# Kernel optimization log

Hardware: AMD Instinct MI355X
Metric: run time of the kernel (lower is better)

Reference implementation:

```python
import jax, jax.numpy as jnp
import numpy as np

B, L, E, H = 4, 2048, 1024, 16
HD = E // H  # 64
ROPE_BASE = 10000.0


def setup_inputs() -> dict:
    key = jax.random.key(0)
    ks = jax.random.split(key, 4)
    x = jax.random.normal(ks[0], (B, L, E), dtype=jnp.float32)
    Wqkv = jax.random.normal(ks[1], (3 * E, E), dtype=jnp.float32) * (E ** -0.5)
    bqkv = jnp.zeros((3 * E,), dtype=jnp.float32)
    Wout = jax.random.normal(ks[2], (E, E), dtype=jnp.float32) * (E ** -0.5)
    bout = jnp.zeros((E,), dtype=jnp.float32)
    # RoPE tables: (1, 1, L, HD/2)
    half = HD // 2
    inv_freq = 1.0 / (ROPE_BASE ** (jnp.arange(half, dtype=jnp.float32) / half))
    t = jnp.arange(L, dtype=jnp.float32)
    freqs = t[:, None] * inv_freq[None, :]  # (L, half)
    cos = jnp.cos(freqs)[None, None]
    sin = jnp.sin(freqs)[None, None]
    return {"x": x, "cos": cos, "sin": sin, "Wqkv": Wqkv, "bqkv": bqkv,
            "Wout": Wout, "bout": bout}


def _apply_rope(q, k, cos, sin):
    half = q.shape[-1] // 2
    q1, q2 = q[..., :half], q[..., half:]
    k1, k2 = k[..., :half], k[..., half:]
    q_rot = jnp.concatenate([q1 * cos - q2 * sin, q1 * sin + q2 * cos], axis=-1)
    k_rot = jnp.concatenate([k1 * cos - k2 * sin, k1 * sin + k2 * cos], axis=-1)
    return q_rot, k_rot


def reference(x, cos, sin, Wqkv, bqkv, Wout, bout):
    b, l, e = x.shape
    qkv = x @ Wqkv.T + bqkv  # (B, L, 3E)
    q, k, v = jnp.split(qkv, 3, axis=-1)
    # (B, H, L, HD)
    q = q.reshape(b, l, H, HD).transpose(0, 2, 1, 3)
    k = k.reshape(b, l, H, HD).transpose(0, 2, 1, 3)
    v = v.reshape(b, l, H, HD).transpose(0, 2, 1, 3)
    q, k = _apply_rope(q, k, cos, sin)
    scale = 1.0 / jnp.sqrt(jnp.asarray(HD, dtype=x.dtype))
    scores = jnp.einsum('bhqd,bhkd->bhqk', q, k) * scale
    attn = jax.nn.softmax(scores, axis=-1)
    out = jnp.einsum('bhqk,bhkd->bhqd', attn, v)  # (B, H, L, HD)
    out = out.transpose(0, 2, 1, 3).reshape(b, l, e)
    out = out @ Wout.T + bout
    return out
```

## Files before the change

### kernel.cpp

```cpp
#include <hip/hip_runtime.h>
#include <math.h>

#define B 4
#define L 2048
#define E 1024
#define H 16
#define HD 64
#define MROWS (B*L)
#define E3 (3*E)

using bf16x8   = __attribute__((ext_vector_type(8))) short;
using f16x8    = __attribute__((ext_vector_type(8))) _Float16;
using floatx4  = __attribute__((ext_vector_type(4))) float;
using floatx16 = __attribute__((ext_vector_type(16))) float;

__device__ inline ushort f2bf(float x) {
    uint u = __float_as_uint(x);
    u += 0x7FFF + ((u >> 16) & 1);
    return (ushort)(u >> 16);
}
__device__ inline float bf2f(ushort h) { return __uint_as_float(((uint)h) << 16); }
__device__ inline ushort f2h(float x) { _Float16 h = (_Float16)x; return *(ushort*)&h; }

#if __has_builtin(__builtin_amdgcn_exp2f)
#define EXP2F(x) __builtin_amdgcn_exp2f(x)
#else
#define EXP2F(x) exp2f(x)
#endif

__device__ inline void async16(const void* g, void* l) {
    __builtin_amdgcn_global_load_lds(
        (const __attribute__((address_space(1))) uint*)g,
        (__attribute__((address_space(3))) uint*)l, 16, 0, 0);
}

__device__ inline uint pack_rtz(float odd, float even) {
    return __builtin_amdgcn_perm(__float_as_uint(odd), __float_as_uint(even), 0x07060302u);
}

#define VMW(n)  asm volatile("s_waitcnt vmcnt(" #n ")" ::: "memory")
#define LGKM0() asm volatile("s_waitcnt lgkmcnt(0)" ::: "memory")
#define SBAR()  __builtin_amdgcn_s_barrier()
#define SCHED0() __builtin_amdgcn_sched_barrier(0)

#define N1Q ((size_t)MROWS * E / 4)
#define N2Q ((size_t)E3 * E / 4)
#define N3Q ((size_t)E * E / 4)
__global__ __launch_bounds__(256) void cvt_all(
        const float* __restrict__ x, const float* __restrict__ wq,
        const float* __restrict__ wo, ushort* __restrict__ x16,
        ushort* __restrict__ wq16, ushort* __restrict__ wo16)
{
    size_t i = (size_t)blockIdx.x * 256 + threadIdx.x;
    const float* src; ushort* dst; size_t j;
    if (i < N1Q)                  { src = x;  dst = x16;  j = i; }
    else if (i < N1Q + N2Q)       { src = wq; dst = wq16; j = i - N1Q; }
    else                          { src = wo; dst = wo16; j = i - N1Q - N2Q; }
    float4 v = ((const float4*)src)[j];
    ushort4 o;
    o.x = f2h(v.x); o.y = f2h(v.y); o.z = f2h(v.z); o.w = f2h(v.w);
    ((ushort4*)dst)[j] = o;
}

template<int MODE>
__global__ __launch_bounds__(256, 2) void gemm4w(
        const ushort* __restrict__ A16, const ushort* __restrict__ B16,
        const float* __restrict__ bias, float* __restrict__ Cf,
        ushort* __restrict__ qh, ushort* __restrict__ kh, ushort* __restrict__ vT,
        const float* __restrict__ cosT, const float* __restrict__ sinT,
        int Ndim, int Kdim)
{
    constexpr int BM    = 256;
    constexpr int ACOLS = BM * 32;
    constexpr int SLOT  = ACOLS + 4096;
    __shared__ ushort lds[3][SLOT];

    const int tid  = threadIdx.x;
    const int w    = tid >> 6, lane = tid & 63;
    const int g    = lane >> 4, c = lane & 15;
    const int wm   = w >> 1,  wn = w & 1;

    const int gx  = gridDim.x;
    const int nwg = gx * gridDim.y;
    int bid = blockIdx.y * gx + blockIdx.x;
    bid = (bid & 7) * (nwg >> 3) + (bid >> 3);
    const int m0 = (bid / gx) * BM;
    const int n0 = (bid % gx) * 128;

    const int rl = lane >> 2, q = lane & 3;
    const ushort* srcA[4]; int dstA[4];
#pragma unroll
    for (int p = 0; p < 4; ++p) {
        const int row = (w * 4 + p) * 16 + rl;
        const int kg  = q ^ ((row >> 1) & 3);
        srcA[p] = A16 + (size_t)(m0 + row) * Kdim + kg * 8;
        dstA[p] = (w * 4 + p) * 512;
    }
    const ushort* srcB[2]; int dstB[2];
#pragma unroll
    for (int p = 0; p < 2; ++p) {
        const int n  = (w * 2 + p) * 16 + rl;
        const int kg = q ^ ((n >> 1) & 3);
        srcB[p] = B16 + (size_t)(n0 + n) * Kdim + kg * 8;
        dstB[p] = ACOLS + (w * 2 + p) * 512;
    }

    auto stageA = [&](ushort* base) {
#pragma unroll
        for (int p = 0; p < 4; ++p) { async16(srcA[p], base + dstA[p]); srcA[p] += 32; }
    };
    auto stageB = [&](ushort* base) {
#pragma unroll
        for (int p = 0; p < 2; ++p) { async16(srcB[p], base + dstB[p]); srcB[p] += 32; }
    };

    floatx4 acc[8][4];
#pragma unroll
    for (int m = 0; m < 8; ++m)
#pragma unroll
        for (int n = 0; n < 4; ++n) acc[m][n] = (floatx4){0.f, 0.f, 0.f, 0.f};

    const int swz   = (g ^ ((c >> 1) & 3)) << 3;
    const int baseA = (wm * 128 + c) * 32 + swz;
    const int baseB = ACOLS + (wn * 64 + c) * 32 + swz;

    const int NKH = Kdim >> 5;

    stageA(&lds[0][0]); stageB(&lds[0][0]);
    stageA(&lds[1][0]); stageB(&lds[1][0]);
    VMW(6);
    SBAR();

    int cs = 0, ts = 2;
    for (int h = 0; h < NKH; ++h) {
        const ushort* cur = &lds[cs][0];
        const bool pre = (h + 2 < NKH);
        f16x8 af[8], bf[4];

#pragma unroll
        for (int m = 0; m < 4; ++m) af[m] = *(const f16x8*)&cur[baseA + m * 512];
#pragma unroll
        for (int n = 0; n < 4; ++n) bf[n] = *(const f16x8*)&cur[baseB + n * 512];
        if (pre) stageA(&lds[ts][0]);
        SBAR();
        LGKM0();
        SCHED0();
        __builtin_amdgcn_s_setprio(1);
#pragma unroll
        for (int m = 0; m < 4; ++m)
#pragma unroll
            for (int n = 0; n < 4; ++n)
                acc[m][n] = __builtin_amdgcn_mfma_f32_16x16x32_f16(af[m], bf[n], acc[m][n], 0, 0, 0);
        __builtin_amdgcn_s_setprio(0);
        SBAR();

#pragma unroll
        for (int m = 4; m < 8; ++m) af[m] = *(const f16x8*)&cur[baseA + m * 512];
        if (pre) { stageB(&lds[ts][0]); VMW(6); }
        else if (h == NKH - 2) { VMW(0); }
        SBAR();
        LGKM0();
        SCHED0();
        __builtin_amdgcn_s_setprio(1);
#pragma unroll
        for (int m = 4; m < 8; ++m)
#pragma unroll
            for (int n = 0; n < 4; ++n)
                acc[m][n] = __builtin_amdgcn_mfma_f32_16x16x32_f16(af[m], bf[n], acc[m][n], 0, 0, 0);
        __builtin_amdgcn_s_setprio(0);
        SBAR();

        cs = (cs == 2) ? 0 : cs + 1;
        ts = (ts == 2) ? 0 : ts + 1;
    }

    const int colbase = n0 + wn * 64;
#pragma unroll
    for (int fm = 0; fm < 8; ++fm) {
        const int rowb = m0 + wm * 128 + fm * 16 + g * 4;
        if constexpr (MODE == 2) {
#pragma unroll
            for (int i = 0; i < 4; ++i) {
                const int row = rowb + i;
#pragma unroll
                for (int nt = 0; nt < 4; ++nt) {
                    const int col = colbase + nt * 16 + c;
                    Cf[(size_t)row * Ndim + col] = acc[fm][nt][i] + bias[col];
                }
            }
        } else {
            const int sec = colbase >> 10;
            const int hg  = (colbase & 1023) >> 6;
#pragma unroll
            for (int i = 0; i < 4; ++i) {
                const int row = rowb + i;
                const int bb = row >> 11;
                const int l  = row & (L - 1);
                if (sec < 2) {
                    ushort* dst = (sec == 0 ? qh : kh) + ((size_t)(bb * H + hg) * L + l) * HD;
                    const int sw = l & 7;
                    const float qs = (sec == 0) ? 0.18033688f : 1.0f;
#pragma unroll
                    for (int nt = 0; nt < 2; ++nt) {
                        const int d  = nt * 16 + c;
                        const int d2 = d + 32;
                        float v1 = acc[fm][nt][i]     + bias[colbase + d];
                        float v2 = acc[fm][nt + 2][i] + bias[colbase + d2];
                        float cs2 = cosT[l * 32 + d], sn = sinT[l * 32 + d];
                        dst[(((d  >> 3) ^ sw) << 3) | (d  & 7)] = f2bf((v1 * cs2 - v2 * sn) * qs);
                        dst[(((d2 >> 3) ^ sw) << 3) | (d2 & 7)] = f2bf((v1 * sn + v2 * cs2) * qs);
                    }
                } else {
                    const int lp = (l & ~12) | ((l & 4) << 1) | ((l & 8) >> 1);
                    const int intile = ((((lp >> 3) & 7)) << 3);
#pragma unroll
                    for (int nt = 0; nt < 4; ++nt) {
                        const int d = nt * 16 + c;
                        float v = acc[fm][nt][i] + bias[colbase + d];
                        size_t idx = ((size_t)(bb * H + hg) * HD + d) * L
                                   + (l & ~63) + (intile ^ ((d & 7) << 3)) + (lp & 7);
                        vT[idx] = f2bf(v);
                    }
                }
            }
        }
    }
}

__global__ __launch_bounds__(256, 4) void flash_mfma4(
        const ushort* __restrict__ qh, const ushort* __restrict__ kh,
        const ushort* __restrict__ vT, ushort* __restrict__ attn16)
{
    __shared__ ushort Ks[2][4096];
    __shared__ ushort Vt[2][4096];

    const int tid  = threadIdx.x;
    const int w    = tid >> 6;
    const int lane = tid & 63;
    const int h    = lane >> 5;
    const int n    = lane & 31;
    const int b    = blockIdx.x >> 4;
    const int hd   = blockIdx.x & 15;
    const int q0   = blockIdx.y * 128;

    const ushort* khead = kh + (size_t)(b * H + hd) * L * HD;
    const ushort* vhead = vT + (size_t)(b * H + hd) * HD * L;

    const int q = q0 + 32 * w + n;
    const ushort* qrow = qh + ((size_t)(b * H + hd) * L + q) * HD;
    bf16x8 aq[4];
#pragma unroll
    for (int kd = 0; kd < 4; ++kd)
        aq[kd] = *(const bf16x8*)&qrow[((2 * kd + h) ^ (q & 7)) << 3];

    const int wk = w & 1;
    const ushort* ksrc = khead + (size_t)(32 * wk) * 64 + lane * 8;
    const ushort* vsrc = vhead + (size_t)(32 * wk + (lane >> 3)) * L + (lane & 7) * 8;

    const int NIT = L / 64;
    if (w < 2) {
#pragma unroll
        for (int p = 0; p < 4; ++p)
            async16(ksrc + p * 512, &Ks[0][32 * wk * 64 + p * 512]);
    } else {
#pragma unroll
        for (int p = 0; p < 4; ++p)
            async16(vsrc + (size_t)p * 8 * L, &Vt[0][32 * wk * 64 + p * 512]);
    }

    float l_i = 0.f;
    floatx16 o[2];
    o[0] = (floatx16)(0.f);
    o[1] = (floatx16)(0.f);

    for (int it = 0; it < NIT; ++it) {
        const int p = it & 1;
        __syncthreads();

        if (it + 1 < NIT) {
            if (w < 2) {
                const ushort* s = ksrc + (size_t)(it + 1) * 4096;
#pragma unroll
                for (int pp = 0; pp < 4; ++pp)
                    async16(s + pp * 512, &Ks[p ^ 1][32 * wk * 64 + pp * 512]);
            } else {
                const ushort* s = vsrc + (size_t)(it + 1) * 64;
#pragma unroll
                for (int pp = 0; pp < 4; ++pp)
                    async16(s + (size_t)pp * 8 * L, &Vt[p ^ 1][32 * wk * 64 + pp * 512]);
            }
        }

        const ushort* KsC = Ks[p];
        const ushort* VtC = Vt[p];

#pragma unroll
        for (int js = 0; js < 2; ++js) {
            floatx16 s = (floatx16)(-16.0f);
#pragma unroll
            for (int kd = 0; kd < 4; ++kd) {
                bf16x8 kf = *(const bf16x8*)&KsC[(32 * js + n) * 64 + (((2 * kd + h) ^ (n & 7)) << 3)];
                s = __builtin_amdgcn_mfma_f32_32x32x16_bf16(kf, aq[kd], s, 0, 0, 0);
            }

            float pv[16];
            float rs = 0.f;
#pragma unroll
            for (int rr = 0; rr < 4; ++rr) {
                float p0 = EXP2F(s[4 * rr + 0]);
                float p1 = EXP2F(s[4 * rr + 1]);
                float p2 = EXP2F(s[4 * rr + 2]);
                float p3 = EXP2F(s[4 * rr + 3]);
                pv[4 * rr + 0] = p0; pv[4 * rr + 1] = p1;
                pv[4 * rr + 2] = p2; pv[4 * rr + 3] = p3;
                rs += (p0 + p1) + (p2 + p3);
            }
            l_i += rs;

#pragma unroll
            for (int f = 0; f < 2; ++f) {
                uint bu[4];
                bu[0] = pack_rtz(pv[8 * f + 1], pv[8 * f + 0]);
                bu[1] = pack_rtz(pv[8 * f + 3], pv[8 * f + 2]);
                bu[2] = pack_rtz(pv[8 * f + 5], pv[8 * f + 4]);
                bu[3] = pack_rtz(pv[8 * f + 7], pv[8 * f + 6]);
                bf16x8 bp = *(const bf16x8*)&bu[0];
#pragma unroll
                for (int nt = 0; nt < 2; ++nt) {
                    bf16x8 vf = *(const bf16x8*)&VtC[(32 * nt + n) * 64 + (((4 * js + 2 * f + h) ^ (n & 7)) << 3)];
                    o[nt] = __builtin_amdgcn_mfma_f32_32x32x16_bf16(vf, bp, o[nt], 0, 0, 0);
                }
            }
        }
    }

    const float l_tot = l_i + __shfl_xor(l_i, 32, 64);
    const float inv = 1.f / l_tot;
    const size_t rowbase = ((size_t)(b * L + q)) * E + hd * HD;
#pragma unroll
    for (int nt = 0; nt < 2; ++nt)
#pragma unroll
        for (int rr = 0; rr < 4; ++rr) {
            const int d0 = 32 * nt + 8 * rr + 4 * h;
            ushort h0 = f2h(o[nt][4 * rr + 0] * inv);
            ushort h1 = f2h(o[nt][4 * rr + 1] * inv);
            ushort h2 = f2h(o[nt][4 * rr + 2] * inv);
            ushort h3 = f2h(o[nt][4 * rr + 3] * inv);
            uint2 hw;
            hw.x = (uint)h0 | ((uint)h1 << 16);
            hw.y = (uint)h2 | ((uint)h3 << 16);
            *(uint2*)&attn16[rowbase + d0] = hw;
        }
}

extern "C" void kernel_launch(void* const* d_in, const int* in_sizes, int n_in,
                              void* d_out, int out_size, void* d_ws, size_t ws_size,
                              hipStream_t stream) {
    const float* x    = (const float*)d_in[0];
    const float* cosT = (const float*)d_in[1];
    const float* sinT = (const float*)d_in[2];
    const float* Wqkv = (const float*)d_in[3];
    const float* bqkv = (const float*)d_in[4];
    const float* Wout = (const float*)d_in[5];
    const float* bout = (const float*)d_in[6];
    float* out = (float*)d_out;

    const size_t NX = (size_t)MROWS * E;
    ushort* us   = (ushort*)d_ws;
    ushort* qh   = us;
    ushort* kh   = us + NX;
    ushort* vTp  = us + 2 * NX;
    ushort* x16  = us + 3 * NX;
    ushort* at16 = us + 4 * NX;
    ushort* wq16 = us + 5 * NX;
    ushort* wo16 = wq16 + (size_t)E3 * E;

    const int cvt_blocks = (int)((N1Q + N2Q + N3Q + 255) / 256);
    cvt_all<<<cvt_blocks, 256, 0, stream>>>(x, Wqkv, Wout, x16, wq16, wo16);

    gemm4w<1><<<dim3(E3 / 128, MROWS / 256), 256, 0, stream>>>(
        x16, wq16, bqkv, nullptr, qh, kh, vTp, cosT, sinT, E3, E);

    flash_mfma4<<<dim3(B * H, L / 128), 256, 0, stream>>>(qh, kh, vTp, at16);

    gemm4w<2><<<dim3(E / 128, MROWS / 256), 256, 0, stream>>>(
        at16, wo16, bout, out, nullptr, nullptr, nullptr, nullptr, nullptr, E, E);
}
```

Measured before the change: 293.1 us.

## Double-buffer GEMM register fragments to overlap LDS reads with MFMA

Restructures the GEMM main loop into a software-pipelined form. The loop is unrolled by two and ping-pongs between two register fragment sets, so the LDS reads for the next k-step are issued before the MFMAs of the current step. Global-to-LDS staging now happens once per k-step, and each step uses a single barrier instead of four. This is meant to hide LDS latency and cut synchronisation. The cost is higher register pressure from holding two fragment sets, which may lower occupancy, and the waitcnt accounting (lgkmcnt(12)) becomes delicate.

```diff
diff --git a/kernel.cpp b/kernel.cpp
--- a/kernel.cpp
+++ b/kernel.cpp
@@ -38,9 +38,10 @@
     return __builtin_amdgcn_perm(__float_as_uint(odd), __float_as_uint(even), 0x07060302u);
 }
 
-#define VMW(n)  asm volatile("s_waitcnt vmcnt(" #n ")" ::: "memory")
-#define LGKM0() asm volatile("s_waitcnt lgkmcnt(0)" ::: "memory")
-#define SBAR()  __builtin_amdgcn_s_barrier()
+#define VMW(n)   asm volatile("s_waitcnt vmcnt(" #n ")" ::: "memory")
+#define LGKM12() asm volatile("s_waitcnt lgkmcnt(12)" ::: "memory")
+#define LGKM0()  asm volatile("s_waitcnt lgkmcnt(0)" ::: "memory")
+#define SBAR()   __builtin_amdgcn_s_barrier()
 #define SCHED0() __builtin_amdgcn_sched_barrier(0)
 
 #define N1Q ((size_t)MROWS * E / 4)
@@ -105,11 +106,9 @@
         dstB[p] = ACOLS + (w * 2 + p) * 512;
     }
 
-    auto stageA = [&](ushort* base) {
+    auto stage = [&](ushort* base) {
 #pragma unroll
         for (int p = 0; p < 4; ++p) { async16(srcA[p], base + dstA[p]); srcA[p] += 32; }
-    };
-    auto stageB = [&](ushort* base) {
 #pragma unroll
         for (int p = 0; p < 2; ++p) { async16(srcB[p], base + dstB[p]); srcB[p] += 32; }
     };
@@ -124,55 +123,69 @@
     const int baseA = (wm * 128 + c) * 32 + swz;
     const int baseB = ACOLS + (wn * 64 + c) * 32 + swz;
 
+#define LOADFRAGS(AF, BF, SL) do {                                        \
+    const ushort* _b = &lds[SL][0];                                       \
+    _Pragma("unroll")                                                     \
+    for (int _m = 0; _m < 8; ++_m) AF[_m] = *(const f16x8*)&_b[baseA + _m * 512]; \
+    _Pragma("unroll")                                                     \
+    for (int _n = 0; _n < 4; ++_n) BF[_n] = *(const f16x8*)&_b[baseB + _n * 512]; \
+} while (0)
+
+#define MFMA32(AF, BF) do {                                               \
+    __builtin_amdgcn_s_setprio(1);                                        \
+    _Pragma("unroll")                                                     \
+    for (int _m = 0; _m < 8; ++_m)                                        \
+    _Pragma("unroll")                                                     \
+    for (int _n = 0; _n < 4; ++_n)                                        \
+        acc[_m][_n] = __builtin_amdgcn_mfma_f32_16x16x32_f16(AF[_m], BF[_n], acc[_m][_n], 0, 0, 0); \
+    __builtin_amdgcn_s_setprio(0);                                        \
+} while (0)
+
     const int NKH = Kdim >> 5;
 
-    stageA(&lds[0][0]); stageB(&lds[0][0]);
-    stageA(&lds[1][0]); stageB(&lds[1][0]);
+    f16x8 af0[8], bf0[4], af1[8], bf1[4];
+
+    stage(&lds[0][0]);
+    stage(&lds[1][0]);
     VMW(6);
     SBAR();
-
-    int cs = 0, ts = 2;
-    for (int h = 0; h < NKH; ++h) {
-        const ushort* cur = &lds[cs][0];
-        const bool pre = (h + 2 < NKH);
-        f16x8 af[8], bf[4];
-
-#pragma unroll
-        for (int m = 0; m < 4; ++m) af[m] = *(const f16x8*)&cur[baseA + m * 512];
-#pragma unroll
-        for (int n = 0; n < 4; ++n) bf[n] = *(const f16x8*)&cur[baseB + n * 512];
-        if (pre) stageA(&lds[ts][0]);
-        SBAR();
-        LGKM0();
-        SCHED0();
-        __builtin_amdgcn_s_setprio(1);
-#pragma unroll
-        for (int m = 0; m < 4; ++m)
-#pragma unroll
-            for (int n = 0; n < 4; ++n)
-                acc[m][n] = __builtin_amdgcn_mfma_f32_16x16x32_f16(af[m], bf[n], acc[m][n], 0, 0, 0);
-        __builtin_amdgcn_s_setprio(0);
-        SBAR();
-
-#pragma unroll
-        for (int m = 4; m < 8; ++m) af[m] = *(const f16x8*)&cur[baseA + m * 512];
-        if (pre) { stageB(&lds[ts][0]); VMW(6); }
-        else if (h == NKH - 2) { VMW(0); }
-        SBAR();
-        LGKM0();
-        SCHED0();
-        __builtin_amdgcn_s_setprio(1);
-#pragma unroll
-        for (int m = 4; m < 8; ++m)
-#pragma unroll
-            for (int n = 0; n < 4; ++n)
-                acc[m][n] = __builtin_amdgcn_mfma_f32_16x16x32_f16(af[m], bf[n], acc[m][n], 0, 0, 0);
-        __builtin_amdgcn_s_setprio(0);
-        SBAR();
-
-        cs = (cs == 2) ? 0 : cs + 1;
-        ts = (ts == 2) ? 0 : ts + 1;
-    }
+    SCHED0();
+    LOADFRAGS(af0, bf0, 0);
+
+    int rs = 1, ts = 2;
+    for (int hh = 0; hh < NKH; hh += 2) {
+        {
+            const bool st = (hh + 2 < NKH);
+            if (st) stage(&lds[ts][0]);
+            if (st) { VMW(6); } else { VMW(0); }
+            SBAR();
+            SCHED0();
+            LOADFRAGS(af1, bf1, rs);
+            LGKM12();
+            SCHED0();
+            MFMA32(af0, bf0);
+            rs = (rs == 2) ? 0 : rs + 1;
+            ts = (ts == 2) ? 0 : ts + 1;
+        }
+        {
+            const int h = hh + 1;
+            const bool st = (h + 2 < NKH);
+            const bool rd = (h + 1 < NKH);
+            if (st) stage(&lds[ts][0]);
+            if (st) { VMW(6); } else { VMW(0); }
+            SBAR();
+            SCHED0();
+            if (rd) { LOADFRAGS(af0, bf0, rs); LGKM12(); }
+            else    { LGKM0(); }
+            SCHED0();
+            MFMA32(af1, bf1);
+            rs = (rs == 2) ? 0 : rs + 1;
+            ts = (ts == 2) ? 0 : ts + 1;
+        }
+    }
+
+#undef LOADFRAGS
+#undef MFMA32
 
     const int colbase = n0 + wn * 64;
 #pragma unroll
```

After: 303.6 us. 3.6% more time.

## Replace GEMM with 8-wave 256x256 tile kernel using ping-pong LDS pipeline

Applied to the files above, without the earlier changes.

Rewrites the projection GEMM kernel to use 512 threads (8 waves as 2x4) computing a 256x256 output tile with K-step 64, double-buffered LDS of 128KB and a finer-grained interleave of half-tile async loads with quarter MFMA blocks. The larger tile raises arithmetic intensity per LDS/global byte and halves the grid. It trades occupancy (one block per CU) and fewer workgroups (e.g. 128 blocks for the output projection) for reuse, risking under-filled CUs on the smaller GEMM.

```diff
diff --git a/kernel.cpp b/kernel.cpp
--- a/kernel.cpp
+++ b/kernel.cpp
@@ -38,9 +38,9 @@
     return __builtin_amdgcn_perm(__float_as_uint(odd), __float_as_uint(even), 0x07060302u);
 }
 
-#define VMW(n)  asm volatile("s_waitcnt vmcnt(" #n ")" ::: "memory")
-#define LGKM0() asm volatile("s_waitcnt lgkmcnt(0)" ::: "memory")
-#define SBAR()  __builtin_amdgcn_s_barrier()
+#define VMW(n)   asm volatile("s_waitcnt vmcnt(" #n ")" ::: "memory")
+#define LGKM0()  asm volatile("s_waitcnt lgkmcnt(0)" ::: "memory")
+#define SBAR()   __builtin_amdgcn_s_barrier()
 #define SCHED0() __builtin_amdgcn_sched_barrier(0)
 
 #define N1Q ((size_t)MROWS * E / 4)
@@ -63,55 +63,44 @@
 }
 
 template<int MODE>
-__global__ __launch_bounds__(256, 2) void gemm4w(
+__global__ __launch_bounds__(512, 1) void gemm8p(
         const ushort* __restrict__ A16, const ushort* __restrict__ B16,
         const float* __restrict__ bias, float* __restrict__ Cf,
         ushort* __restrict__ qh, ushort* __restrict__ kh, ushort* __restrict__ vT,
         const float* __restrict__ cosT, const float* __restrict__ sinT,
         int Ndim, int Kdim)
 {
-    constexpr int BM    = 256;
-    constexpr int ACOLS = BM * 32;
-    constexpr int SLOT  = ACOLS + 4096;
-    __shared__ ushort lds[3][SLOT];
+    __shared__ ushort lds[65536];
 
     const int tid  = threadIdx.x;
     const int w    = tid >> 6, lane = tid & 63;
     const int g    = lane >> 4, c = lane & 15;
-    const int wm   = w >> 1,  wn = w & 1;
+    const int wm   = w >> 2,  wn = w & 3;
 
     const int gx  = gridDim.x;
     const int nwg = gx * gridDim.y;
     int bid = blockIdx.y * gx + blockIdx.x;
     bid = (bid & 7) * (nwg >> 3) + (bid >> 3);
-    const int m0 = (bid / gx) * BM;
-    const int n0 = (bid % gx) * 128;
-
-    const int rl = lane >> 2, q = lane & 3;
-    const ushort* srcA[4]; int dstA[4];
-#pragma unroll
-    for (int p = 0; p < 4; ++p) {
-        const int row = (w * 4 + p) * 16 + rl;
-        const int kg  = q ^ ((row >> 1) & 3);
-        srcA[p] = A16 + (size_t)(m0 + row) * Kdim + kg * 8;
-        dstA[p] = (w * 4 + p) * 512;
-    }
-    const ushort* srcB[2]; int dstB[2];
-#pragma unroll
-    for (int p = 0; p < 2; ++p) {
-        const int n  = (w * 2 + p) * 16 + rl;
-        const int kg = q ^ ((n >> 1) & 3);
-        srcB[p] = B16 + (size_t)(n0 + n) * Kdim + kg * 8;
-        dstB[p] = ACOLS + (w * 2 + p) * 512;
-    }
-
-    auto stageA = [&](ushort* base) {
-#pragma unroll
-        for (int p = 0; p < 4; ++p) { async16(srcA[p], base + dstA[p]); srcA[p] += 32; }
+    const int m0 = (bid / gx) * 256;
+    const int n0 = (bid % gx) * 256;
+
+    const int srow = tid >> 3;
+    const int gsrc = (tid & 7) ^ ((tid >> 3) & 7);
+    const ushort* pA = A16 + (size_t)(m0 + srow) * Kdim + gsrc * 8;
+    const ushort* pB = B16 + (size_t)(n0 + srow) * Kdim + gsrc * 8;
+    const int dst8 = tid << 3;
+
+    auto stageA = [&](int d, int hf, int kt) {
+#pragma unroll
+        for (int p = 0; p < 2; ++p)
+            async16(pA + (size_t)(hf * 128 + p * 64) * Kdim + kt * 64,
+                    &lds[d * 32768 + hf * 8192 + p * 4096 + dst8]);
     };
-    auto stageB = [&](ushort* base) {
-#pragma unroll
-        for (int p = 0; p < 2; ++p) { async16(srcB[p], base + dstB[p]); srcB[p] += 32; }
+    auto stageB = [&](int d, int hf, int kt) {
+#pragma unroll
+        for (int p = 0; p < 2; ++p)
+            async16(pB + (size_t)(hf * 128 + p * 64) * Kdim + kt * 64,
+                    &lds[d * 32768 + 16384 + hf * 8192 + p * 4096 + dst8]);
     };
 
     floatx4 acc[8][4];
@@ -120,59 +109,99 @@
 #pragma unroll
         for (int n = 0; n < 4; ++n) acc[m][n] = (floatx4){0.f, 0.f, 0.f, 0.f};
 
-    const int swz   = (g ^ ((c >> 1) & 3)) << 3;
-    const int baseA = (wm * 128 + c) * 32 + swz;
-    const int baseB = ACOLS + (wn * 64 + c) * 32 + swz;
-
-    const int NKH = Kdim >> 5;
-
-    stageA(&lds[0][0]); stageB(&lds[0][0]);
-    stageA(&lds[1][0]); stageB(&lds[1][0]);
+    const int kg0 = (g ^ (c & 7)) << 3;
+
+#define LDA4(AR, FL, D) do {                                               \
+    const int _ab = (D) * 32768 + wm * 8192 + (FL) * 4096 + c * 64;        \
+    _Pragma("unroll")                                                      \
+    for (int _f = 0; _f < 4; ++_f) {                                       \
+        AR[_f][0] = *(const f16x8*)&lds[_ab + _f * 1024 + kg0];            \
+        AR[_f][1] = *(const f16x8*)&lds[_ab + _f * 1024 + (kg0 ^ 32)];     \
+    } } while (0)
+
+#define LDB2(BR, NL, D) do {                                               \
+    const int _bb = (D) * 32768 + 16384 + (wn >> 1) * 8192                 \
+                  + ((wn & 1) * 64 + c) * 64 + (NL) * 2048;                \
+    _Pragma("unroll")                                                      \
+    for (int _j = 0; _j < 2; ++_j) {                                       \
+        BR[_j][0] = *(const f16x8*)&lds[_bb + _j * 1024 + kg0];            \
+        BR[_j][1] = *(const f16x8*)&lds[_bb + _j * 1024 + (kg0 ^ 32)];     \
+    } } while (0)
+
+#define QMFMA(AR, BR, MO, NO) do {                                         \
+    __builtin_amdgcn_s_setprio(1);                                         \
+    _Pragma("unroll")                                                      \
+    for (int _f = 0; _f < 4; ++_f)                                         \
+    _Pragma("unroll")                                                      \
+    for (int _j = 0; _j < 2; ++_j) {                                       \
+        acc[(MO)+_f][(NO)+_j] = __builtin_amdgcn_mfma_f32_16x16x32_f16(    \
+            AR[_f][0], BR[_j][0], acc[(MO)+_f][(NO)+_j], 0, 0, 0);         \
+        acc[(MO)+_f][(NO)+_j] = __builtin_amdgcn_mfma_f32_16x16x32_f16(    \
+            AR[_f][1], BR[_j][1], acc[(MO)+_f][(NO)+_j], 0, 0, 0);         \
+    }                                                                      \
+    __builtin_amdgcn_s_setprio(0);                                         \
+} while (0)
+
+    f16x8 a0[4][2], a1[4][2], b0[2][2], b1[2][2];
+
+    const int NI = Kdim >> 7;
+
+    stageA(0, 0, 0); stageB(0, 0, 0); stageB(0, 1, 0);
+    stageA(0, 1, 0); stageB(1, 0, 1); stageB(1, 1, 1);
     VMW(6);
     SBAR();
 
-    int cs = 0, ts = 2;
-    for (int h = 0; h < NKH; ++h) {
-        const ushort* cur = &lds[cs][0];
-        const bool pre = (h + 2 < NKH);
-        f16x8 af[8], bf[4];
-
-#pragma unroll
-        for (int m = 0; m < 4; ++m) af[m] = *(const f16x8*)&cur[baseA + m * 512];
-#pragma unroll
-        for (int n = 0; n < 4; ++n) bf[n] = *(const f16x8*)&cur[baseB + n * 512];
-        if (pre) stageA(&lds[ts][0]);
-        SBAR();
-        LGKM0();
-        SCHED0();
-        __builtin_amdgcn_s_setprio(1);
-#pragma unroll
-        for (int m = 0; m < 4; ++m)
-#pragma unroll
-            for (int n = 0; n < 4; ++n)
-                acc[m][n] = __builtin_amdgcn_mfma_f32_16x16x32_f16(af[m], bf[n], acc[m][n], 0, 0, 0);
-        __builtin_amdgcn_s_setprio(0);
-        SBAR();
-
-#pragma unroll
-        for (int m = 4; m < 8; ++m) af[m] = *(const f16x8*)&cur[baseA + m * 512];
-        if (pre) { stageB(&lds[ts][0]); VMW(6); }
-        else if (h == NKH - 2) { VMW(0); }
-        SBAR();
-        LGKM0();
-        SCHED0();
-        __builtin_amdgcn_s_setprio(1);
-#pragma unroll
-        for (int m = 4; m < 8; ++m)
-#pragma unroll
-            for (int n = 0; n < 4; ++n)
-                acc[m][n] = __builtin_amdgcn_mfma_f32_16x16x32_f16(af[m], bf[n], acc[m][n], 0, 0, 0);
-        __builtin_amdgcn_s_setprio(0);
-        SBAR();
-
-        cs = (cs == 2) ? 0 : cs + 1;
-        ts = (ts == 2) ? 0 : ts + 1;
+    for (int it = 0; it < NI; ++it) {
+        const int kt1 = 2 * it + 1, kt2 = 2 * it + 2, kt3 = 2 * it + 3;
+        const bool pre = (it + 1 < NI);
+
+        VMW(6);
+        LDA4(a0, 0, 0); LDB2(b0, 0, 0);
+        stageA(1, 0, kt1);
+        SBAR(); LGKM0(); SCHED0();
+        QMFMA(a0, b0, 0, 0);
+        SBAR();
+        LDB2(b1, 1, 0);
+        stageA(1, 1, kt1);
+        SBAR(); LGKM0(); SCHED0();
+        QMFMA(a0, b1, 0, 2);
+        SBAR();
+        VMW(6);
+        LDA4(a1, 1, 0);
+        if (pre) stageB(0, 0, kt2);
+        SBAR(); LGKM0(); SCHED0();
+        QMFMA(a1, b1, 4, 2);
+        SBAR();
+        if (pre) stageB(0, 1, kt2);
+        SBAR(); LGKM0(); SCHED0();
+        QMFMA(a1, b0, 4, 0);
+        SBAR();
+        VMW(6);
+        LDA4(a0, 0, 1); LDB2(b0, 0, 1);
+        if (pre) stageA(0, 0, kt2);
+        SBAR(); LGKM0(); SCHED0();
+        QMFMA(a0, b0, 0, 0);
+        SBAR();
+        LDB2(b1, 1, 1);
+        if (pre) stageA(0, 1, kt2);
+        SBAR(); LGKM0(); SCHED0();
+        QMFMA(a0, b1, 0, 2);
+        SBAR();
+        VMW(6);
+        LDA4(a1, 1, 1);
+        if (pre) stageB(1, 0, kt3);
+        SBAR(); LGKM0(); SCHED0();
+        QMFMA(a1, b1, 4, 2);
+        SBAR();
+        if (pre) stageB(1, 1, kt3);
+        SBAR(); LGKM0(); SCHED0();
+        QMFMA(a1, b0, 4, 0);
+        SBAR();
     }
+
+#undef LDA4
+#undef LDB2
+#undef QMFMA
 
     const int colbase = n0 + wn * 64;
 #pragma unroll
@@ -378,11 +407,11 @@
     const int cvt_blocks = (int)((N1Q + N2Q + N3Q + 255) / 256);
     cvt_all<<<cvt_blocks, 256, 0, stream>>>(x, Wqkv, Wout, x16, wq16, wo16);
 
-    gemm4w<1><<<dim3(E3 / 128, MROWS / 256), 256, 0, stream>>>(
+    gemm8p<1><<<dim3(E3 / 256, MROWS / 256), 512, 0, stream>>>(
         x16, wq16, bqkv, nullptr, qh, kh, vTp, cosT, sinT, E3, E);
 
     flash_mfma4<<<dim3(B * H, L / 128), 256, 0, stream>>>(qh, kh, vTp, at16);
 
-    gemm4w<2><<<dim3(E / 128, MROWS / 256), 256, 0, stream>>>(
+    gemm8p<2><<<dim3(E / 256, MROWS / 256), 512, 0, stream>>>(
         at16, wo16, bout, out, nullptr, nullptr, nullptr, nullptr, nullptr, E, E);
 }
```

Measured after the change: 293.8 us. About the same (+0.2%).
